# Kernel tuning notes

Hardware: AMD Instinct MI355X
Metric: run time of the kernel (lower is better)

Reference implementation:

```python
import jax, jax.numpy as jnp
import numpy as np
import math

IN_FEATURES = 1024
OUT_FEATURES = 1024
N_BANK = 8192
N_LAYER = 12
N_EMBD = 1024


def setup_inputs() -> dict:
    key = jax.random.key(0)
    kq, kk, kv = jax.random.split(key, 3)
    q = jax.random.normal(kq, (4, 2048, IN_FEATURES), dtype=jnp.float32)
    k = 0.02 * jax.random.normal(kk, (N_BANK, IN_FEATURES), dtype=jnp.float32)
    v_std = 2.0 / N_LAYER / math.sqrt(N_EMBD)
    v = v_std * jax.random.normal(kv, (N_BANK, OUT_FEATURES), dtype=jnp.float32)
    return {"q": q, "k": k, "v": v}


def reference(q, k, v):
    # scores: [B, T, N]
    scores = jnp.einsum("btd,nd->btn", q, k)
    # row-wise L2 normalization, scaled by sqrt(N), then exact (erf) GELU
    sqrt_n = jnp.sqrt(jnp.asarray(scores.shape[-1], scores.dtype))
    norm = jnp.linalg.norm(scores, axis=-1, keepdims=True)
    gated = jax.nn.gelu(scores / norm * sqrt_n, approximate=False)
    # out: [B, T, out_features]
    return jnp.einsum("btn,no->bto", gated, v)
```

## Files before the change

kernel.cpp:

```cpp
#include <hip/hip_runtime.h>
#include <hip/hip_bf16.h>
#include <math.h>


#define MROWS 8192
#define DIN   1024
#define NBANK 8192
#define DOUT  1024

typedef float  f32x4  __attribute__((ext_vector_type(4)));
typedef __bf16 bf16x8 __attribute__((ext_vector_type(8)));

__device__ __forceinline__ float bf2f(unsigned short u) {
  union { unsigned int i; float f; } x; x.i = ((unsigned int)u) << 16; return x.f;
}
__device__ __forceinline__ unsigned short f2bf(float f) {
  union { float f; unsigned int i; } x; x.f = f;
  unsigned int u = x.i;
  unsigned int r = (u + 0x7fffu + ((u >> 16) & 1u)) >> 16;
  return (unsigned short)r;
}

__global__ void cvt_kernel(const float* __restrict__ src,
                           unsigned short* __restrict__ dst, int n) {
  int i = (blockIdx.x * 256 + threadIdx.x) * 4;
  if (i >= n) return;
  float4 vv = *(const float4*)(src + i);
  ushort4 o;
  o.x = f2bf(vv.x); o.y = f2bf(vv.y); o.z = f2bf(vv.z); o.w = f2bf(vv.w);
  *(ushort4*)(dst + i) = o;
}

__global__ void transpose_cvt_kernel(const float* __restrict__ src,
                                     unsigned short* __restrict__ dst,
                                     int R, int C) {
  __shared__ float tile[32][33];
  int c0 = blockIdx.x * 32, r0 = blockIdx.y * 32;
  for (int i = threadIdx.y; i < 32; i += 8)
    tile[i][threadIdx.x] = src[(size_t)(r0 + i) * C + c0 + threadIdx.x];
  __syncthreads();
  for (int i = threadIdx.y; i < 32; i += 8)
    dst[(size_t)(c0 + i) * R + r0 + threadIdx.x] = f2bf(tile[threadIdx.x][i]);
}

__global__ void zero_f32_kernel(float* __restrict__ p, int n4) {
  int i = blockIdx.x * 256 + threadIdx.x;
  if (i < n4) ((float4*)p)[i] = make_float4(0.f, 0.f, 0.f, 0.f);
}

__global__ __launch_bounds__(256, 2) void gemm1_kernel(
    const unsigned short* __restrict__ A, const unsigned short* __restrict__ B,
    unsigned short* __restrict__ C, float* __restrict__ sumsq) {
  __shared__ unsigned short As[128 * 32];
  __shared__ unsigned short Bs[128 * 32];
  const int K = DIN, ldc = NBANK;

  const int tid  = threadIdx.x;
  const int lane = tid & 63;
  const int wave = tid >> 6;
  const int wm   = (wave >> 1) * 64;
  const int wn   = (wave & 1) * 64;
  const int quad = lane >> 4;
  const int l16  = lane & 15;

  const int flat = blockIdx.y * gridDim.x + blockIdx.x;
  const int nwg  = gridDim.x * gridDim.y;
  const int swz  = (flat & 7) * (nwg >> 3) + (flat >> 3);
  const size_t m0 = (size_t)(swz / gridDim.x) * 128;
  const size_t n0 = (size_t)(swz % gridDim.x) * 128;

  const int srow = tid >> 2;
  const int scol = (tid & 3) * 8;
  const unsigned short* Ag0 = A + (m0 + srow) * (size_t)K + scol;
  const unsigned short* Ag1 = A + (m0 + srow + 64) * (size_t)K + scol;
  const unsigned short* Bg0 = B + (n0 + srow) * (size_t)K + scol;
  const unsigned short* Bg1 = B + (n0 + srow + 64) * (size_t)K + scol;

  unsigned short* AsW0 = As + tid * 8;
  unsigned short* AsW1 = As + 64 * 32 + tid * 8;
  unsigned short* BsW0 = Bs + tid * 8;
  unsigned short* BsW1 = Bs + 64 * 32 + tid * 8;

  const unsigned short* ArP = As + (wm + l16) * 32 + quad * 8;
  const unsigned short* BrP = Bs + (wn + l16) * 32 + quad * 8;

  f32x4 acc[4][4];
#pragma unroll
  for (int i = 0; i < 4; i++)
#pragma unroll
    for (int j = 0; j < 4; j++) {
      f32x4 z = {0.f, 0.f, 0.f, 0.f};
      acc[i][j] = z;
    }

  for (int k0 = 0; k0 < K; k0 += 32) {
    __builtin_amdgcn_global_load_lds(
        (const __attribute__((address_space(1))) unsigned int*)(Ag0 + k0),
        (__attribute__((address_space(3))) unsigned int*)AsW0, 16, 0, 0);
    __builtin_amdgcn_global_load_lds(
        (const __attribute__((address_space(1))) unsigned int*)(Ag1 + k0),
        (__attribute__((address_space(3))) unsigned int*)AsW1, 16, 0, 0);
    __builtin_amdgcn_global_load_lds(
        (const __attribute__((address_space(1))) unsigned int*)(Bg0 + k0),
        (__attribute__((address_space(3))) unsigned int*)BsW0, 16, 0, 0);
    __builtin_amdgcn_global_load_lds(
        (const __attribute__((address_space(1))) unsigned int*)(Bg1 + k0),
        (__attribute__((address_space(3))) unsigned int*)BsW1, 16, 0, 0);
    __syncthreads();

    bf16x8 af[4], bfr[4];
#pragma unroll
    for (int i = 0; i < 4; i++) af[i] = *(const bf16x8*)(ArP + i * 16 * 32);
#pragma unroll
    for (int j = 0; j < 4; j++) bfr[j] = *(const bf16x8*)(BrP + j * 16 * 32);
#pragma unroll
    for (int i = 0; i < 4; i++)
#pragma unroll
      for (int j = 0; j < 4; j++)
        acc[i][j] = __builtin_amdgcn_mfma_f32_16x16x32_bf16(af[i], bfr[j],
                                                            acc[i][j], 0, 0, 0);
    __syncthreads();
  }

#pragma unroll
  for (int i = 0; i < 4; i++)
#pragma unroll
    for (int r = 0; r < 4; r++) {
      size_t row = m0 + wm + i * 16 + quad * 4 + r;
      float s = 0.f;
#pragma unroll
      for (int j = 0; j < 4; j++) {
        float val = acc[i][j][r];
        s += val * val;
        C[row * (size_t)ldc + n0 + wn + j * 16 + l16] = f2bf(val);
      }
      s += __shfl_xor(s, 1);
      s += __shfl_xor(s, 2);
      s += __shfl_xor(s, 4);
      s += __shfl_xor(s, 8);
      if (l16 == 0) atomicAdd(&sumsq[row], s);
    }
}

__global__ void gelu_kernel(unsigned short* __restrict__ S,
                            const float* __restrict__ sumsq) {
  const size_t total = (size_t)MROWS * NBANK / 8;
  for (size_t u = (size_t)blockIdx.x * 256 + threadIdx.x; u < total;
       u += (size_t)gridDim.x * 256) {
    size_t idx = u * 8;
    int row = (int)(idx >> 13);
    float sc = sqrtf((float)NBANK / sumsq[row]);
    uint4 vv = *(const uint4*)(S + idx);
    unsigned int w[4] = {vv.x, vv.y, vv.z, vv.w};
#pragma unroll
    for (int e = 0; e < 4; e++) {
      float x0 = bf2f((unsigned short)(w[e] & 0xffffu)) * sc;
      float x1 = bf2f((unsigned short)(w[e] >> 16)) * sc;
      float g0 = 0.5f * x0 * (1.0f + erff(x0 * 0.70710678118654752f));
      float g1 = 0.5f * x1 * (1.0f + erff(x1 * 0.70710678118654752f));
      w[e] = (unsigned int)f2bf(g0) | ((unsigned int)f2bf(g1) << 16);
    }
    uint4 o; o.x = w[0]; o.y = w[1]; o.z = w[2]; o.w = w[3];
    *(uint4*)(S + idx) = o;
  }
}

__global__ __launch_bounds__(512, 4) void gemm2_kernel(
    const unsigned short* __restrict__ A,
    const unsigned short* __restrict__ B,
    float* __restrict__ C) {
  __shared__ unsigned short As[128 * 32];
  __shared__ unsigned short Bs[256 * 32];
  const int K = NBANK, ldc = DOUT;

  const int tid  = threadIdx.x;
  const int lane = tid & 63;
  const int wave = tid >> 6;
  const int wm   = (wave >> 2) * 64;
  const int wn   = (wave & 3) * 64;
  const int quad = lane >> 4;
  const int l16  = lane & 15;

  const int flat = blockIdx.y * gridDim.x + blockIdx.x;
  const int nwg  = gridDim.x * gridDim.y;
  const int swz  = (flat & 7) * (nwg >> 3) + (flat >> 3);
  const size_t m0 = (size_t)(swz / gridDim.x) * 128;
  const size_t n0 = (size_t)(swz % gridDim.x) * 256;
  const int    ks = blockIdx.z * (K / 2);

  const int srow = tid >> 2;
  const int scol = (tid & 3) * 8;
  const unsigned short* Ag  = A + (m0 + srow) * (size_t)K + scol + ks;
  const unsigned short* Bg0 = B + (n0 + srow) * (size_t)K + scol + ks;
  const unsigned short* Bg1 = B + (n0 + srow + 128) * (size_t)K + scol + ks;

  unsigned short* AsW  = As + tid * 8;
  unsigned short* BsW0 = Bs + tid * 8;
  unsigned short* BsW1 = Bs + 512 * 8 + tid * 8;

  const unsigned short* ArP = As + (wm + l16) * 32 + quad * 8;
  const unsigned short* BrP = Bs + (wn + l16) * 32 + quad * 8;

  f32x4 acc[4][4];
#pragma unroll
  for (int i = 0; i < 4; i++)
#pragma unroll
    for (int j = 0; j < 4; j++) {
      f32x4 z = {0.f, 0.f, 0.f, 0.f};
      acc[i][j] = z;
    }

  for (int k0 = 0; k0 < K / 2; k0 += 32) {
    __builtin_amdgcn_global_load_lds(
        (const __attribute__((address_space(1))) unsigned int*)(Ag + k0),
        (__attribute__((address_space(3))) unsigned int*)AsW, 16, 0, 0);
    __builtin_amdgcn_global_load_lds(
        (const __attribute__((address_space(1))) unsigned int*)(Bg0 + k0),
        (__attribute__((address_space(3))) unsigned int*)BsW0, 16, 0, 0);
    __builtin_amdgcn_global_load_lds(
        (const __attribute__((address_space(1))) unsigned int*)(Bg1 + k0),
        (__attribute__((address_space(3))) unsigned int*)BsW1, 16, 0, 0);
    __syncthreads();

    bf16x8 af[4], bfr[4];
#pragma unroll
    for (int i = 0; i < 4; i++) af[i] = *(const bf16x8*)(ArP + i * 16 * 32);
#pragma unroll
    for (int j = 0; j < 4; j++) bfr[j] = *(const bf16x8*)(BrP + j * 16 * 32);
#pragma unroll
    for (int i = 0; i < 4; i++)
#pragma unroll
      for (int j = 0; j < 4; j++)
        acc[i][j] = __builtin_amdgcn_mfma_f32_16x16x32_bf16(af[i], bfr[j],
                                                            acc[i][j], 0, 0, 0);
    __syncthreads();
  }

#pragma unroll
  for (int i = 0; i < 4; i++)
#pragma unroll
    for (int j = 0; j < 4; j++)
#pragma unroll
      for (int r = 0; r < 4; r++) {
        size_t row = m0 + wm + i * 16 + quad * 4 + r;
        size_t col = n0 + wn + j * 16 + l16;
        atomicAdd(&C[row * (size_t)ldc + col], acc[i][j][r]);
      }
}

extern "C" void kernel_launch(void* const* d_in, const int* in_sizes, int n_in,
                              void* d_out, int out_size, void* d_ws, size_t ws_size,
                              hipStream_t stream) {
  const float* q = (const float*)d_in[0];
  const float* k = (const float*)d_in[1];
  const float* v = (const float*)d_in[2];
  float* out = (float*)d_out;

  char* ws = (char*)d_ws;
  const size_t MB = 1024ull * 1024ull;
  unsigned short* qb     = (unsigned short*)(ws);
  unsigned short* kb     = (unsigned short*)(ws + 16 * MB);
  unsigned short* vbT    = (unsigned short*)(ws + 32 * MB);
  unsigned short* scores = (unsigned short*)(ws + 48 * MB);
  float*          scale  = (float*)(ws + 176 * MB);

  const int nqk = MROWS * DIN;

  zero_f32_kernel<<<(MROWS * DOUT / 4 + 255) / 256, 256, 0, stream>>>(out,
                                                                      MROWS * DOUT / 4);
  zero_f32_kernel<<<(MROWS / 4 + 255) / 256, 256, 0, stream>>>(scale, MROWS / 4);

  cvt_kernel<<<nqk / 1024, 256, 0, stream>>>(q, qb, nqk);
  cvt_kernel<<<nqk / 1024, 256, 0, stream>>>(k, kb, nqk);
  transpose_cvt_kernel<<<dim3(DOUT / 32, NBANK / 32), dim3(32, 8), 0, stream>>>(
      v, vbT, NBANK, DOUT);

  gemm1_kernel<<<dim3(NBANK / 128, MROWS / 128), 256, 0, stream>>>(qb, kb, scores,
                                                                   scale);

  gelu_kernel<<<4096, 256, 0, stream>>>(scores, scale);

  gemm2_kernel<<<dim3(DOUT / 256, MROWS / 128, 2), 512, 0, stream>>>(scores, vbT, out);
}
```

Baseline: 614.0 us.

## Share a double-buffered 256x256 pipelined GEMM core between both matmuls

Replaces both GEMM kernels with a shared core that computes 256x256 tiles using 8 waves, a K-step of 64, and double-buffered LDS. Global-to-LDS prefetch of the next tile is interleaved with MFMA phases using explicit waitcnt, barriers and setprio. The goal is to overlap memory latency with matrix work and raise arithmetic intensity per loaded byte. The cost is 128KB of LDS per block, which lowers occupancy and leaves fewer blocks (256 for gemm2) to fill the CUs.

```diff
diff --git a/kernel.cpp b/kernel.cpp
--- a/kernel.cpp
+++ b/kernel.cpp
@@ -48,91 +48,157 @@
   if (i < n4) ((float4*)p)[i] = make_float4(0.f, 0.f, 0.f, 0.f);
 }
 
-__global__ __launch_bounds__(256, 2) void gemm1_kernel(
+
+__device__ __forceinline__ void stage_half(const unsigned short* src, int ld,
+                                           unsigned short* dstbase, int tid) {
+  __builtin_amdgcn_global_load_lds(
+      (const __attribute__((address_space(1))) unsigned int*)src,
+      (__attribute__((address_space(3))) unsigned int*)(dstbase + tid * 8), 16, 0, 0);
+  __builtin_amdgcn_global_load_lds(
+      (const __attribute__((address_space(1))) unsigned int*)(src + (size_t)128 * ld),
+      (__attribute__((address_space(3))) unsigned int*)(dstbase + 4096 + tid * 8), 16,
+      0, 0);
+}
+
+__device__ __forceinline__ void read4(const unsigned short* base, bf16x8 f[4]) {
+#pragma unroll
+  for (int i = 0; i < 4; ++i) f[i] = *(const bf16x8*)(base + i * 512);
+}
+
+__device__ __forceinline__ void mfma16(const bf16x8 a[4], const bf16x8 b[4],
+                                       f32x4 (&acc)[8][4], int mh) {
+#pragma unroll
+  for (int m = 0; m < 4; ++m)
+#pragma unroll
+    for (int n = 0; n < 4; ++n)
+      acc[mh * 4 + m][n] = __builtin_amdgcn_mfma_f32_16x16x32_bf16(
+          a[m], b[n], acc[mh * 4 + m][n], 0, 0, 0);
+}
+
+__device__ __forceinline__ void gemm_core(const unsigned short* __restrict__ Ap,
+                                          const unsigned short* __restrict__ Bp,
+                                          int lda, int ldb, int nkt,
+                                          unsigned short* As, unsigned short* Bs,
+                                          f32x4 (&acc)[8][4]) {
+  const int tid  = threadIdx.x;
+  const int lane = tid & 63;
+  const int wm   = (tid >> 6) >> 2;
+  const int wn   = (tid >> 6) & 3;
+  const int quad = lane >> 4;
+  const int l16  = lane & 15;
+  const int aoff = (wm * 128 + l16) * 32 + quad * 8;
+  const int boff = (wn * 64 + l16) * 32 + quad * 8;
+
+  const unsigned short* Ag = Ap + (size_t)(tid >> 2) * lda + (tid & 3) * 8;
+  const unsigned short* Bg = Bp + (size_t)(tid >> 2) * ldb + (tid & 3) * 8;
+
+#pragma unroll
+  for (int i = 0; i < 8; ++i)
+#pragma unroll
+    for (int j = 0; j < 4; ++j) {
+      f32x4 z = {0.f, 0.f, 0.f, 0.f};
+      acc[i][j] = z;
+    }
+
+  stage_half(Ag, lda, As, tid);
+  stage_half(Bg, ldb, Bs, tid);
+  stage_half(Ag + 32, lda, As + 8192, tid);
+  stage_half(Bg + 32, ldb, Bs + 8192, tid);
+  asm volatile("s_waitcnt vmcnt(4)" ::: "memory");
+  __builtin_amdgcn_s_barrier();
+
+  for (int kt = 0; kt < nkt; ++kt) {
+    const int cur = kt & 1, nx = cur ^ 1;
+    const unsigned short* Ab = As + cur * 16384;
+    const unsigned short* Bb = Bs + cur * 16384;
+    unsigned short* Asn = As + nx * 16384;
+    unsigned short* Bsn = Bs + nx * 16384;
+    const bool pf = (kt + 1 < nkt);
+    const int knext = (kt + 1) * 64;
+    bf16x8 a[4], b[4];
+
+    read4(Ab + aoff, a);
+    read4(Bb + boff, b);
+    if (pf) stage_half(Ag + knext, lda, Asn, tid);
+    __builtin_amdgcn_s_barrier();
+    asm volatile("s_waitcnt lgkmcnt(0)" ::: "memory");
+    __builtin_amdgcn_sched_barrier(0);
+    __builtin_amdgcn_s_setprio(1);
+    mfma16(a, b, acc, 0);
+    __builtin_amdgcn_s_setprio(0);
+    __builtin_amdgcn_s_barrier();
+
+    read4(Ab + aoff + 2048, a);
+    if (pf) stage_half(Bg + knext, ldb, Bsn, tid);
+    __builtin_amdgcn_s_barrier();
+    asm volatile("s_waitcnt lgkmcnt(0)" ::: "memory");
+    __builtin_amdgcn_sched_barrier(0);
+    __builtin_amdgcn_s_setprio(1);
+    mfma16(a, b, acc, 1);
+    __builtin_amdgcn_s_setprio(0);
+    if (pf)
+      asm volatile("s_waitcnt vmcnt(4)" ::: "memory");
+    else
+      asm volatile("s_waitcnt vmcnt(0)" ::: "memory");
+    __builtin_amdgcn_s_barrier();
+
+    read4(Ab + 8192 + aoff + 2048, a);
+    read4(Bb + 8192 + boff, b);
+    if (pf) stage_half(Ag + knext + 32, lda, Asn + 8192, tid);
+    __builtin_amdgcn_s_barrier();
+    asm volatile("s_waitcnt lgkmcnt(0)" ::: "memory");
+    __builtin_amdgcn_sched_barrier(0);
+    __builtin_amdgcn_s_setprio(1);
+    mfma16(a, b, acc, 1);
+    __builtin_amdgcn_s_setprio(0);
+    __builtin_amdgcn_s_barrier();
+
+    read4(Ab + 8192 + aoff, a);
+    if (pf) stage_half(Bg + knext + 32, ldb, Bsn + 8192, tid);
+    __builtin_amdgcn_s_barrier();
+    asm volatile("s_waitcnt lgkmcnt(0)" ::: "memory");
+    __builtin_amdgcn_sched_barrier(0);
+    __builtin_amdgcn_s_setprio(1);
+    mfma16(a, b, acc, 0);
+    __builtin_amdgcn_s_setprio(0);
+    if (pf) asm volatile("s_waitcnt vmcnt(4)" ::: "memory");
+    __builtin_amdgcn_s_barrier();
+  }
+}
+
+__global__ __launch_bounds__(512) void gemm1_kernel(
     const unsigned short* __restrict__ A, const unsigned short* __restrict__ B,
     unsigned short* __restrict__ C, float* __restrict__ sumsq) {
-  __shared__ unsigned short As[128 * 32];
-  __shared__ unsigned short Bs[128 * 32];
-  const int K = DIN, ldc = NBANK;
-
-  const int tid  = threadIdx.x;
-  const int lane = tid & 63;
-  const int wave = tid >> 6;
-  const int wm   = (wave >> 1) * 64;
-  const int wn   = (wave & 1) * 64;
-  const int quad = lane >> 4;
-  const int l16  = lane & 15;
+  __shared__ unsigned short As[2 * 16384];
+  __shared__ unsigned short Bs[2 * 16384];
 
   const int flat = blockIdx.y * gridDim.x + blockIdx.x;
   const int nwg  = gridDim.x * gridDim.y;
   const int swz  = (flat & 7) * (nwg >> 3) + (flat >> 3);
-  const size_t m0 = (size_t)(swz / gridDim.x) * 128;
-  const size_t n0 = (size_t)(swz % gridDim.x) * 128;
-
-  const int srow = tid >> 2;
-  const int scol = (tid & 3) * 8;
-  const unsigned short* Ag0 = A + (m0 + srow) * (size_t)K + scol;
-  const unsigned short* Ag1 = A + (m0 + srow + 64) * (size_t)K + scol;
-  const unsigned short* Bg0 = B + (n0 + srow) * (size_t)K + scol;
-  const unsigned short* Bg1 = B + (n0 + srow + 64) * (size_t)K + scol;
-
-  unsigned short* AsW0 = As + tid * 8;
-  unsigned short* AsW1 = As + 64 * 32 + tid * 8;
-  unsigned short* BsW0 = Bs + tid * 8;
-  unsigned short* BsW1 = Bs + 64 * 32 + tid * 8;
-
-  const unsigned short* ArP = As + (wm + l16) * 32 + quad * 8;
-  const unsigned short* BrP = Bs + (wn + l16) * 32 + quad * 8;
-
-  f32x4 acc[4][4];
-#pragma unroll
-  for (int i = 0; i < 4; i++)
-#pragma unroll
-    for (int j = 0; j < 4; j++) {
-      f32x4 z = {0.f, 0.f, 0.f, 0.f};
-      acc[i][j] = z;
-    }
-
-  for (int k0 = 0; k0 < K; k0 += 32) {
-    __builtin_amdgcn_global_load_lds(
-        (const __attribute__((address_space(1))) unsigned int*)(Ag0 + k0),
-        (__attribute__((address_space(3))) unsigned int*)AsW0, 16, 0, 0);
-    __builtin_amdgcn_global_load_lds(
-        (const __attribute__((address_space(1))) unsigned int*)(Ag1 + k0),
-        (__attribute__((address_space(3))) unsigned int*)AsW1, 16, 0, 0);
-    __builtin_amdgcn_global_load_lds(
-        (const __attribute__((address_space(1))) unsigned int*)(Bg0 + k0),
-        (__attribute__((address_space(3))) unsigned int*)BsW0, 16, 0, 0);
-    __builtin_amdgcn_global_load_lds(
-        (const __attribute__((address_space(1))) unsigned int*)(Bg1 + k0),
-        (__attribute__((address_space(3))) unsigned int*)BsW1, 16, 0, 0);
-    __syncthreads();
-
-    bf16x8 af[4], bfr[4];
-#pragma unroll
-    for (int i = 0; i < 4; i++) af[i] = *(const bf16x8*)(ArP + i * 16 * 32);
-#pragma unroll
-    for (int j = 0; j < 4; j++) bfr[j] = *(const bf16x8*)(BrP + j * 16 * 32);
-#pragma unroll
-    for (int i = 0; i < 4; i++)
-#pragma unroll
-      for (int j = 0; j < 4; j++)
-        acc[i][j] = __builtin_amdgcn_mfma_f32_16x16x32_bf16(af[i], bfr[j],
-                                                            acc[i][j], 0, 0, 0);
-    __syncthreads();
-  }
-
-#pragma unroll
-  for (int i = 0; i < 4; i++)
-#pragma unroll
-    for (int r = 0; r < 4; r++) {
-      size_t row = m0 + wm + i * 16 + quad * 4 + r;
+  const size_t m0 = (size_t)(swz / gridDim.x) * 256;
+  const size_t n0 = (size_t)(swz % gridDim.x) * 256;
+
+  f32x4 acc[8][4];
+  gemm_core(A + m0 * DIN, B + n0 * DIN, DIN, DIN, DIN / 64, As, Bs, acc);
+
+  const int tid  = threadIdx.x;
+  const int lane = tid & 63;
+  const int wm   = (tid >> 6) >> 2;
+  const int wn   = (tid >> 6) & 3;
+  const int quad = lane >> 4;
+  const int l16  = lane & 15;
+
+#pragma unroll
+  for (int mf = 0; mf < 8; ++mf)
+#pragma unroll
+    for (int r = 0; r < 4; ++r) {
+      size_t row = m0 + wm * 128 + mf * 16 + quad * 4 + r;
       float s = 0.f;
 #pragma unroll
-      for (int j = 0; j < 4; j++) {
-        float val = acc[i][j][r];
+      for (int nf = 0; nf < 4; ++nf) {
+        float val = acc[mf][nf][r];
         s += val * val;
-        C[row * (size_t)ldc + n0 + wn + j * 16 + l16] = f2bf(val);
+        C[row * (size_t)NBANK + n0 + wn * 64 + nf * 16 + l16] = f2bf(val);
       }
       s += __shfl_xor(s, 1);
       s += __shfl_xor(s, 2);
@@ -165,86 +231,40 @@
   }
 }
 
-__global__ __launch_bounds__(512, 4) void gemm2_kernel(
+__global__ __launch_bounds__(512) void gemm2_kernel(
     const unsigned short* __restrict__ A,
     const unsigned short* __restrict__ B,
     float* __restrict__ C) {
-  __shared__ unsigned short As[128 * 32];
-  __shared__ unsigned short Bs[256 * 32];
-  const int K = NBANK, ldc = DOUT;
-
-  const int tid  = threadIdx.x;
-  const int lane = tid & 63;
-  const int wave = tid >> 6;
-  const int wm   = (wave >> 2) * 64;
-  const int wn   = (wave & 3) * 64;
-  const int quad = lane >> 4;
-  const int l16  = lane & 15;
+  __shared__ unsigned short As[2 * 16384];
+  __shared__ unsigned short Bs[2 * 16384];
 
   const int flat = blockIdx.y * gridDim.x + blockIdx.x;
   const int nwg  = gridDim.x * gridDim.y;
   const int swz  = (flat & 7) * (nwg >> 3) + (flat >> 3);
-  const size_t m0 = (size_t)(swz / gridDim.x) * 128;
+  const size_t m0 = (size_t)(swz / gridDim.x) * 256;
   const size_t n0 = (size_t)(swz % gridDim.x) * 256;
-  const int    ks = blockIdx.z * (K / 2);
-
-  const int srow = tid >> 2;
-  const int scol = (tid & 3) * 8;
-  const unsigned short* Ag  = A + (m0 + srow) * (size_t)K + scol + ks;
-  const unsigned short* Bg0 = B + (n0 + srow) * (size_t)K + scol + ks;
-  const unsigned short* Bg1 = B + (n0 + srow + 128) * (size_t)K + scol + ks;
-
-  unsigned short* AsW  = As + tid * 8;
-  unsigned short* BsW0 = Bs + tid * 8;
-  unsigned short* BsW1 = Bs + 512 * 8 + tid * 8;
-
-  const unsigned short* ArP = As + (wm + l16) * 32 + quad * 8;
-  const unsigned short* BrP = Bs + (wn + l16) * 32 + quad * 8;
-
-  f32x4 acc[4][4];
-#pragma unroll
-  for (int i = 0; i < 4; i++)
-#pragma unroll
-    for (int j = 0; j < 4; j++) {
-      f32x4 z = {0.f, 0.f, 0.f, 0.f};
-      acc[i][j] = z;
-    }
-
-  for (int k0 = 0; k0 < K / 2; k0 += 32) {
-    __builtin_amdgcn_global_load_lds(
-        (const __attribute__((address_space(1))) unsigned int*)(Ag + k0),
-        (__attribute__((address_space(3))) unsigned int*)AsW, 16, 0, 0);
-    __builtin_amdgcn_global_load_lds(
-        (const __attribute__((address_space(1))) unsigned int*)(Bg0 + k0),
-        (__attribute__((address_space(3))) unsigned int*)BsW0, 16, 0, 0);
-    __builtin_amdgcn_global_load_lds(
-        (const __attribute__((address_space(1))) unsigned int*)(Bg1 + k0),
-        (__attribute__((address_space(3))) unsigned int*)BsW1, 16, 0, 0);
-    __syncthreads();
-
-    bf16x8 af[4], bfr[4];
-#pragma unroll
-    for (int i = 0; i < 4; i++) af[i] = *(const bf16x8*)(ArP + i * 16 * 32);
-#pragma unroll
-    for (int j = 0; j < 4; j++) bfr[j] = *(const bf16x8*)(BrP + j * 16 * 32);
-#pragma unroll
-    for (int i = 0; i < 4; i++)
-#pragma unroll
-      for (int j = 0; j < 4; j++)
-        acc[i][j] = __builtin_amdgcn_mfma_f32_16x16x32_bf16(af[i], bfr[j],
-                                                            acc[i][j], 0, 0, 0);
-    __syncthreads();
-  }
-
-#pragma unroll
-  for (int i = 0; i < 4; i++)
-#pragma unroll
-    for (int j = 0; j < 4; j++)
-#pragma unroll
-      for (int r = 0; r < 4; r++) {
-        size_t row = m0 + wm + i * 16 + quad * 4 + r;
-        size_t col = n0 + wn + j * 16 + l16;
-        atomicAdd(&C[row * (size_t)ldc + col], acc[i][j][r]);
+  const int kbase = blockIdx.z * (NBANK / 2);
+
+  f32x4 acc[8][4];
+  gemm_core(A + m0 * (size_t)NBANK + kbase, B + n0 * (size_t)NBANK + kbase, NBANK,
+            NBANK, (NBANK / 2) / 64, As, Bs, acc);
+
+  const int tid  = threadIdx.x;
+  const int lane = tid & 63;
+  const int wm   = (tid >> 6) >> 2;
+  const int wn   = (tid >> 6) & 3;
+  const int quad = lane >> 4;
+  const int l16  = lane & 15;
+
+#pragma unroll
+  for (int mf = 0; mf < 8; ++mf)
+#pragma unroll
+    for (int nf = 0; nf < 4; ++nf)
+#pragma unroll
+      for (int r = 0; r < 4; ++r) {
+        size_t row = m0 + wm * 128 + mf * 16 + quad * 4 + r;
+        size_t col = n0 + wn * 64 + nf * 16 + l16;
+        atomicAdd(&C[row * (size_t)DOUT + col], acc[mf][nf][r]);
       }
 }
 
@@ -275,10 +295,10 @@
   transpose_cvt_kernel<<<dim3(DOUT / 32, NBANK / 32), dim3(32, 8), 0, stream>>>(
       v, vbT, NBANK, DOUT);
 
-  gemm1_kernel<<<dim3(NBANK / 128, MROWS / 128), 256, 0, stream>>>(qb, kb, scores,
+  gemm1_kernel<<<dim3(NBANK / 256, MROWS / 256), 512, 0, stream>>>(qb, kb, scores,
                                                                    scale);
 
   gelu_kernel<<<4096, 256, 0, stream>>>(scores, scale);
 
-  gemm2_kernel<<<dim3(DOUT / 256, MROWS / 128, 2), 512, 0, stream>>>(scores, vbT, out);
-}
+  gemm2_kernel<<<dim3(DOUT / 256, MROWS / 256, 2), 512, 0, stream>>>(scores, vbT, out);
+}
```

Result: faster. 575.4 us (-6.3%).

## Triple-buffer gemm1 with swizzled LDS and drop gemm2 split-K atomics

Applied to the files above, without the earlier changes.

gemm1 moves to 128x256 tiles with 512 threads and a three-stage LDS ring. Global-to-LDS loads are issued two K-steps ahead and gated by explicit vmcnt waits, MFMA priority is raised, and an XOR swizzle on LDS columns is meant to cut bank conflicts. gemm2 drops split-K and atomics in favour of 128x128 tiles with plain stores and the same swizzle, which also removes the output zeroing kernel. The risks are lower gemm2 parallelism (512 blocks, no K split) and higher LDS and register pressure in gemm1.

```diff
diff --git a/kernel.cpp b/kernel.cpp
--- a/kernel.cpp
+++ b/kernel.cpp
@@ -48,18 +48,18 @@
   if (i < n4) ((float4*)p)[i] = make_float4(0.f, 0.f, 0.f, 0.f);
 }
 
-__global__ __launch_bounds__(256, 2) void gemm1_kernel(
+__global__ __launch_bounds__(512, 4) void gemm1_kernel(
     const unsigned short* __restrict__ A, const unsigned short* __restrict__ B,
     unsigned short* __restrict__ C, float* __restrict__ sumsq) {
-  __shared__ unsigned short As[128 * 32];
-  __shared__ unsigned short Bs[128 * 32];
-  const int K = DIN, ldc = NBANK;
+  __shared__ unsigned short As[3 * 4096];
+  __shared__ unsigned short Bs[3 * 8192];
+  const int K = DIN;
+  const int NKT = DIN / 32;
 
   const int tid  = threadIdx.x;
   const int lane = tid & 63;
-  const int wave = tid >> 6;
-  const int wm   = (wave >> 1) * 64;
-  const int wn   = (wave & 1) * 64;
+  const int wm   = (tid >> 6) >> 2;
+  const int wn   = (tid >> 6) & 3;
   const int quad = lane >> 4;
   const int l16  = lane & 15;
 
@@ -67,22 +67,15 @@
   const int nwg  = gridDim.x * gridDim.y;
   const int swz  = (flat & 7) * (nwg >> 3) + (flat >> 3);
   const size_t m0 = (size_t)(swz / gridDim.x) * 128;
-  const size_t n0 = (size_t)(swz % gridDim.x) * 128;
-
-  const int srow = tid >> 2;
-  const int scol = (tid & 3) * 8;
-  const unsigned short* Ag0 = A + (m0 + srow) * (size_t)K + scol;
-  const unsigned short* Ag1 = A + (m0 + srow + 64) * (size_t)K + scol;
-  const unsigned short* Bg0 = B + (n0 + srow) * (size_t)K + scol;
-  const unsigned short* Bg1 = B + (n0 + srow + 64) * (size_t)K + scol;
-
-  unsigned short* AsW0 = As + tid * 8;
-  unsigned short* AsW1 = As + 64 * 32 + tid * 8;
-  unsigned short* BsW0 = Bs + tid * 8;
-  unsigned short* BsW1 = Bs + 64 * 32 + tid * 8;
-
-  const unsigned short* ArP = As + (wm + l16) * 32 + quad * 8;
-  const unsigned short* BrP = Bs + (wn + l16) * 32 + quad * 8;
+  const size_t n0 = (size_t)(swz % gridDim.x) * 256;
+
+  const int sw   = (l16 >> 1) & 3;
+  const int aoff = (wm * 64 + l16) * 32 + (quad ^ sw) * 8;
+  const int boff = (wn * 64 + l16) * 32 + (quad ^ sw) * 8;
+
+  const int gslot = (tid & 3) ^ ((tid >> 3) & 3);
+  const unsigned short* Ag = A + (m0 + (tid >> 2)) * (size_t)K + gslot * 8;
+  const unsigned short* Bg = B + (n0 + (tid >> 2)) * (size_t)K + gslot * 8;
 
   f32x4 acc[4][4];
 #pragma unroll
@@ -93,46 +86,78 @@
       acc[i][j] = z;
     }
 
-  for (int k0 = 0; k0 < K; k0 += 32) {
-    __builtin_amdgcn_global_load_lds(
-        (const __attribute__((address_space(1))) unsigned int*)(Ag0 + k0),
-        (__attribute__((address_space(3))) unsigned int*)AsW0, 16, 0, 0);
-    __builtin_amdgcn_global_load_lds(
-        (const __attribute__((address_space(1))) unsigned int*)(Ag1 + k0),
-        (__attribute__((address_space(3))) unsigned int*)AsW1, 16, 0, 0);
-    __builtin_amdgcn_global_load_lds(
-        (const __attribute__((address_space(1))) unsigned int*)(Bg0 + k0),
-        (__attribute__((address_space(3))) unsigned int*)BsW0, 16, 0, 0);
-    __builtin_amdgcn_global_load_lds(
-        (const __attribute__((address_space(1))) unsigned int*)(Bg1 + k0),
-        (__attribute__((address_space(3))) unsigned int*)BsW1, 16, 0, 0);
-    __syncthreads();
-
-    bf16x8 af[4], bfr[4];
-#pragma unroll
-    for (int i = 0; i < 4; i++) af[i] = *(const bf16x8*)(ArP + i * 16 * 32);
-#pragma unroll
-    for (int j = 0; j < 4; j++) bfr[j] = *(const bf16x8*)(BrP + j * 16 * 32);
-#pragma unroll
-    for (int i = 0; i < 4; i++)
-#pragma unroll
-      for (int j = 0; j < 4; j++)
-        acc[i][j] = __builtin_amdgcn_mfma_f32_16x16x32_bf16(af[i], bfr[j],
-                                                            acc[i][j], 0, 0, 0);
-    __syncthreads();
+  auto stage = [&](int buf, int koff) {
+    __builtin_amdgcn_global_load_lds(
+        (const __attribute__((address_space(1))) unsigned int*)(Ag + koff),
+        (__attribute__((address_space(3))) unsigned int*)(As + buf * 4096 + tid * 8),
+        16, 0, 0);
+    __builtin_amdgcn_global_load_lds(
+        (const __attribute__((address_space(1))) unsigned int*)(Bg + koff),
+        (__attribute__((address_space(3))) unsigned int*)(Bs + buf * 8192 + tid * 8),
+        16, 0, 0);
+    __builtin_amdgcn_global_load_lds(
+        (const __attribute__((address_space(1))) unsigned int*)(Bg + (size_t)128 * K +
+                                                                koff),
+        (__attribute__((address_space(3))) unsigned int*)(Bs + buf * 8192 + 4096 +
+                                                          tid * 8),
+        16, 0, 0);
+  };
+
+  stage(0, 0);
+  stage(1, 32);
+  asm volatile("s_waitcnt vmcnt(3)" ::: "memory");
+  __builtin_amdgcn_s_barrier();
+  __builtin_amdgcn_sched_barrier(0);
+
+  int cur = 0;
+  for (int t = 0; t < NKT; ++t) {
+    const bool pf = (t + 2) < NKT;
+    if (pf) {
+      int nxt = cur + 2;
+      if (nxt >= 3) nxt -= 3;
+      stage(nxt, (t + 2) * 32);
+    }
+
+    const unsigned short* Ab = As + cur * 4096 + aoff;
+    const unsigned short* Bb = Bs + cur * 8192 + boff;
+    bf16x8 a[4], b[4];
+#pragma unroll
+    for (int i = 0; i < 4; ++i) a[i] = *(const bf16x8*)(Ab + i * 512);
+#pragma unroll
+    for (int j = 0; j < 4; ++j) b[j] = *(const bf16x8*)(Bb + j * 512);
+
+    asm volatile("s_waitcnt lgkmcnt(0)" ::: "memory");
+    __builtin_amdgcn_sched_barrier(0);
+    __builtin_amdgcn_s_setprio(1);
+#pragma unroll
+    for (int i = 0; i < 4; ++i)
+#pragma unroll
+      for (int j = 0; j < 4; ++j)
+        acc[i][j] = __builtin_amdgcn_mfma_f32_16x16x32_bf16(a[i], b[j], acc[i][j],
+                                                            0, 0, 0);
+    __builtin_amdgcn_s_setprio(0);
+
+    if (pf)
+      asm volatile("s_waitcnt vmcnt(3)" ::: "memory");
+    else
+      asm volatile("s_waitcnt vmcnt(0)" ::: "memory");
+    __builtin_amdgcn_s_barrier();
+    __builtin_amdgcn_sched_barrier(0);
+
+    cur = (cur == 2) ? 0 : cur + 1;
   }
 
 #pragma unroll
-  for (int i = 0; i < 4; i++)
-#pragma unroll
-    for (int r = 0; r < 4; r++) {
-      size_t row = m0 + wm + i * 16 + quad * 4 + r;
+  for (int mf = 0; mf < 4; ++mf)
+#pragma unroll
+    for (int r = 0; r < 4; ++r) {
+      size_t row = m0 + wm * 64 + mf * 16 + quad * 4 + r;
       float s = 0.f;
 #pragma unroll
-      for (int j = 0; j < 4; j++) {
-        float val = acc[i][j][r];
+      for (int nf = 0; nf < 4; ++nf) {
+        float val = acc[mf][nf][r];
         s += val * val;
-        C[row * (size_t)ldc + n0 + wn + j * 16 + l16] = f2bf(val);
+        C[row * (size_t)NBANK + n0 + wn * 64 + nf * 16 + l16] = f2bf(val);
       }
       s += __shfl_xor(s, 1);
       s += __shfl_xor(s, 2);
@@ -165,19 +190,19 @@
   }
 }
 
-__global__ __launch_bounds__(512, 4) void gemm2_kernel(
+__global__ __launch_bounds__(256, 4) void gemm2_kernel(
     const unsigned short* __restrict__ A,
     const unsigned short* __restrict__ B,
     float* __restrict__ C) {
   __shared__ unsigned short As[128 * 32];
-  __shared__ unsigned short Bs[256 * 32];
+  __shared__ unsigned short Bs[128 * 32];
   const int K = NBANK, ldc = DOUT;
 
   const int tid  = threadIdx.x;
   const int lane = tid & 63;
   const int wave = tid >> 6;
-  const int wm   = (wave >> 2) * 64;
-  const int wn   = (wave & 3) * 64;
+  const int wm   = (wave >> 1) * 64;
+  const int wn   = (wave & 1) * 64;
   const int quad = lane >> 4;
   const int l16  = lane & 15;
 
@@ -185,21 +210,23 @@
   const int nwg  = gridDim.x * gridDim.y;
   const int swz  = (flat & 7) * (nwg >> 3) + (flat >> 3);
   const size_t m0 = (size_t)(swz / gridDim.x) * 128;
-  const size_t n0 = (size_t)(swz % gridDim.x) * 256;
-  const int    ks = blockIdx.z * (K / 2);
+  const size_t n0 = (size_t)(swz % gridDim.x) * 128;
 
   const int srow = tid >> 2;
-  const int scol = (tid & 3) * 8;
-  const unsigned short* Ag  = A + (m0 + srow) * (size_t)K + scol + ks;
-  const unsigned short* Bg0 = B + (n0 + srow) * (size_t)K + scol + ks;
-  const unsigned short* Bg1 = B + (n0 + srow + 128) * (size_t)K + scol + ks;
-
-  unsigned short* AsW  = As + tid * 8;
+  const int scol = (((tid & 3) ^ ((tid >> 3) & 3))) * 8;
+  const unsigned short* Ag0 = A + (m0 + srow) * (size_t)K + scol;
+  const unsigned short* Ag1 = A + (m0 + srow + 64) * (size_t)K + scol;
+  const unsigned short* Bg0 = B + (n0 + srow) * (size_t)K + scol;
+  const unsigned short* Bg1 = B + (n0 + srow + 64) * (size_t)K + scol;
+
+  unsigned short* AsW0 = As + tid * 8;
+  unsigned short* AsW1 = As + 64 * 32 + tid * 8;
   unsigned short* BsW0 = Bs + tid * 8;
-  unsigned short* BsW1 = Bs + 512 * 8 + tid * 8;
-
-  const unsigned short* ArP = As + (wm + l16) * 32 + quad * 8;
-  const unsigned short* BrP = Bs + (wn + l16) * 32 + quad * 8;
+  unsigned short* BsW1 = Bs + 64 * 32 + tid * 8;
+
+  const int sw = (l16 >> 1) & 3;
+  const unsigned short* ArP = As + (wm + l16) * 32 + (quad ^ sw) * 8;
+  const unsigned short* BrP = Bs + (wn + l16) * 32 + (quad ^ sw) * 8;
 
   f32x4 acc[4][4];
 #pragma unroll
@@ -210,10 +237,13 @@
       acc[i][j] = z;
     }
 
-  for (int k0 = 0; k0 < K / 2; k0 += 32) {
-    __builtin_amdgcn_global_load_lds(
-        (const __attribute__((address_space(1))) unsigned int*)(Ag + k0),
-        (__attribute__((address_space(3))) unsigned int*)AsW, 16, 0, 0);
+  for (int k0 = 0; k0 < K; k0 += 32) {
+    __builtin_amdgcn_global_load_lds(
+        (const __attribute__((address_space(1))) unsigned int*)(Ag0 + k0),
+        (__attribute__((address_space(3))) unsigned int*)AsW0, 16, 0, 0);
+    __builtin_amdgcn_global_load_lds(
+        (const __attribute__((address_space(1))) unsigned int*)(Ag1 + k0),
+        (__attribute__((address_space(3))) unsigned int*)AsW1, 16, 0, 0);
     __builtin_amdgcn_global_load_lds(
         (const __attribute__((address_space(1))) unsigned int*)(Bg0 + k0),
         (__attribute__((address_space(3))) unsigned int*)BsW0, 16, 0, 0);
@@ -244,7 +274,7 @@
       for (int r = 0; r < 4; r++) {
         size_t row = m0 + wm + i * 16 + quad * 4 + r;
         size_t col = n0 + wn + j * 16 + l16;
-        atomicAdd(&C[row * (size_t)ldc + col], acc[i][j][r]);
+        C[row * (size_t)ldc + col] = acc[i][j][r];
       }
 }
 
@@ -266,8 +296,6 @@
 
   const int nqk = MROWS * DIN;
 
-  zero_f32_kernel<<<(MROWS * DOUT / 4 + 255) / 256, 256, 0, stream>>>(out,
-                                                                      MROWS * DOUT / 4);
   zero_f32_kernel<<<(MROWS / 4 + 255) / 256, 256, 0, stream>>>(scale, MROWS / 4);
 
   cvt_kernel<<<nqk / 1024, 256, 0, stream>>>(q, qb, nqk);
@@ -275,10 +303,10 @@
   transpose_cvt_kernel<<<dim3(DOUT / 32, NBANK / 32), dim3(32, 8), 0, stream>>>(
       v, vbT, NBANK, DOUT);
 
-  gemm1_kernel<<<dim3(NBANK / 128, MROWS / 128), 256, 0, stream>>>(qb, kb, scores,
+  gemm1_kernel<<<dim3(NBANK / 256, MROWS / 128), 512, 0, stream>>>(qb, kb, scores,
                                                                    scale);
 
   gelu_kernel<<<4096, 256, 0, stream>>>(scores, scale);
 
-  gemm2_kernel<<<dim3(DOUT / 256, MROWS / 128, 2), 512, 0, stream>>>(scores, vbT, out);
-}
+  gemm2_kernel<<<dim3(DOUT / 128, MROWS / 128), 256, 0, stream>>>(scores, vbT, out);
+}
```

New measurement: 551.0 us. 10.3% less time.
